# Optimization experiments

Hardware: AMD Instinct MI355X
Metric: run time of the kernel (lower is better)

Reference implementation:

```python
import jax, jax.numpy as jnp
import numpy as np

N_NODES = 100000
N_EDGES = 1600000
IN_C, HID_C, OUT_C = 128, 128, 64


def setup_inputs() -> dict:
    key = jax.random.key(0)
    ks = jax.random.split(key, 8)
    x = jax.random.normal(ks[0], (N_NODES, IN_C), dtype=jnp.float32)
    edge_index = jax.random.randint(ks[1], (2, N_EDGES), 0, N_NODES, dtype=jnp.int64)
    # SAGEConv params: lin_l (aggregated neighbors, with bias), lin_r (root, no bias)
    s1 = 1.0 / np.sqrt(IN_C)
    s2 = 1.0 / np.sqrt(HID_C)
    W1_l = jax.random.uniform(ks[2], (IN_C, HID_C), jnp.float32, -s1, s1)
    b1_l = jnp.zeros((HID_C,), jnp.float32)
    W1_r = jax.random.uniform(ks[3], (IN_C, HID_C), jnp.float32, -s1, s1)
    W2_l = jax.random.uniform(ks[4], (HID_C, OUT_C), jnp.float32, -s2, s2)
    b2_l = jnp.zeros((OUT_C,), jnp.float32)
    W2_r = jax.random.uniform(ks[5], (HID_C, OUT_C), jnp.float32, -s2, s2)
    return {"x": x, "edge_index": edge_index, "W1_l": W1_l, "b1_l": b1_l,
            "W1_r": W1_r, "W2_l": W2_l, "b2_l": b2_l, "W2_r": W2_r}


def _sage_conv(x, src, dst, W_l, b_l, W_r):
    # gather source features, scatter-max reduce onto destinations
    msg = x[src]                                             # [E, C]
    aggr = jax.ops.segment_max(msg, dst, num_segments=N_NODES)
    aggr = jnp.where(jnp.isfinite(aggr), aggr, 0.0)          # isolated nodes -> 0 (PyG behavior)
    return aggr @ W_l + b_l + x @ W_r


def reference(x, edge_index, W1_l, b1_l, W1_r, W2_l, b2_l, W2_r):
    src, dst = edge_index[0], edge_index[1]
    h = _sage_conv(x, src, dst, W1_l, b1_l, W1_r)
    h = jax.nn.relu(h)
    # dropout is identity in eval mode
    out = _sage_conv(h, src, dst, W2_l, b2_l, W2_r)
    return out
```

## Files before the change

kernel.cpp:

```cpp
#include <hip/hip_runtime.h>
#include <cstdint>

#define NNODES 100000
#define NEDGES 1600000
#define NBKT   196
#define CAP    9216
#define BIN_CHUNK 4096
#define GBIN ((NEDGES + BIN_CHUNK - 1) / BIN_CHUNK)
#define GCVT (NNODES * 16 / 256)
#define GWPK 24

typedef __attribute__((ext_vector_type(8))) __bf16 bf16x8;
typedef __attribute__((ext_vector_type(4))) float f32x4;
typedef short v2s __attribute__((ext_vector_type(2)));

__device__ __forceinline__ unsigned short f2bf_rne(float f) {
    unsigned int u = __float_as_uint(f);
    u += 0x7fffu + ((u >> 16) & 1u);
    return (unsigned short)(u >> 16);
}
__device__ __forceinline__ unsigned encdec(unsigned u) {
    return u ^ (((u & 0x80008000u) >> 15) * 0x7FFFu);
}
__device__ __forceinline__ unsigned pkmax(unsigned a, unsigned b) {
    v2s r = __builtin_elementwise_max(__builtin_bit_cast(v2s, a), __builtin_bit_cast(v2s, b));
    return __builtin_bit_cast(unsigned, r);
}
__device__ __forceinline__ uint4 pkmax4(uint4 a, uint4 b) {
    uint4 r;
    r.x = pkmax(a.x, b.x); r.y = pkmax(a.y, b.y);
    r.z = pkmax(a.z, b.z); r.w = pkmax(a.w, b.w);
    return r;
}


__global__ __launch_bounds__(256) void prep_kernel(
        const int* __restrict__ src, const int* __restrict__ dst,
        unsigned int* __restrict__ binArr, int* __restrict__ bucketFill,
        const float4* __restrict__ xin, uint4* __restrict__ xeout,
        const float* __restrict__ W1l, const float* __restrict__ W1r,
        const float* __restrict__ W2l, const float* __restrict__ W2r,
        uint4* __restrict__ Wf1, uint4* __restrict__ Wf2, int nE) {
    if (blockIdx.x >= GBIN + GCVT) {
        int t = (blockIdx.x - GBIN - GCVT) * 256 + threadIdx.x;
        unsigned short s[8];
        if (t < 4096) {
            int h = t >> 11, kt = (t >> 9) & 3, nt = (t >> 6) & 7, lane = t & 63;
            const float* W = h ? W1r : W1l;
            int k0 = kt * 32 + (lane >> 4) * 8;
            int col = nt * 16 + (lane & 15);
#pragma unroll
            for (int jj = 0; jj < 8; ++jj) s[jj] = f2bf_rne(W[(k0 + jj) * 128 + col]);
            uint4 o;
            o.x = (unsigned)s[0] | ((unsigned)s[1] << 16);
            o.y = (unsigned)s[2] | ((unsigned)s[3] << 16);
            o.z = (unsigned)s[4] | ((unsigned)s[5] << 16);
            o.w = (unsigned)s[6] | ((unsigned)s[7] << 16);
            Wf1[t] = o;
        } else {
            int u = t - 4096;
            int h = u >> 10, kt = (u >> 8) & 3, nt = (u >> 6) & 3, lane = u & 63;
            const float* W = h ? W2r : W2l;
            int k0 = kt * 32 + (lane >> 4) * 8;
            int col = nt * 16 + (lane & 15);
#pragma unroll
            for (int jj = 0; jj < 8; ++jj) s[jj] = f2bf_rne(W[(k0 + jj) * 64 + col]);
            uint4 o;
            o.x = (unsigned)s[0] | ((unsigned)s[1] << 16);
            o.y = (unsigned)s[2] | ((unsigned)s[3] << 16);
            o.z = (unsigned)s[4] | ((unsigned)s[5] << 16);
            o.w = (unsigned)s[6] | ((unsigned)s[7] << 16);
            Wf2[u] = o;
        }
        return;
    }
    if (blockIdx.x >= GBIN) {
        int t = (blockIdx.x - GBIN) * 256 + threadIdx.x;
        int s = t / (NNODES * 8);
        int rem = t - s * (NNODES * 8);
        int n = rem >> 3, j = rem & 7;
        int f = n * 32 + s * 16 + j * 2;
        float4 v0 = xin[f], v1 = xin[f + 1];
        uint4 o;
        o.x = encdec((unsigned)f2bf_rne(v0.x) | ((unsigned)f2bf_rne(v0.y) << 16));
        o.y = encdec((unsigned)f2bf_rne(v0.z) | ((unsigned)f2bf_rne(v0.w) << 16));
        o.z = encdec((unsigned)f2bf_rne(v1.x) | ((unsigned)f2bf_rne(v1.y) << 16));
        o.w = encdec((unsigned)f2bf_rne(v1.z) | ((unsigned)f2bf_rne(v1.w) << 16));
        xeout[t] = o;
        return;
    }
    __shared__ unsigned int stage[BIN_CHUNK];
    __shared__ unsigned char bof[BIN_CHUNK];
    __shared__ int cnt[256], cstart[256], gbase[256];
    const int tid = threadIdx.x;
    const int blockStart = blockIdx.x * BIN_CHUNK;
    const int chunkN = min(BIN_CHUNK, nE - blockStart);
    cnt[tid] = 0;
    __syncthreads();
    int myd[16], mys[16];
    unsigned short myo[16];
#pragma unroll
    for (int i = 0; i < 16; ++i) {
        int idx = i * 256 + tid;
        if (idx < chunkN) {
            myd[i] = dst[blockStart + idx];
            mys[i] = src[blockStart + idx];
            myo[i] = (unsigned short)atomicAdd(&cnt[myd[i] >> 9], 1);
        }
    }
    __syncthreads();
    int v = cnt[tid];
    for (int off = 1; off < 256; off <<= 1) {
        int add = (tid >= off) ? cnt[tid - off] : 0;
        __syncthreads();
        cnt[tid] += add;
        __syncthreads();
    }
    cstart[tid] = cnt[tid] - v;
    if (tid < NBKT && v > 0) gbase[tid] = atomicAdd(&bucketFill[tid], v);
    __syncthreads();
#pragma unroll
    for (int i = 0; i < 16; ++i) {
        int idx = i * 256 + tid;
        if (idx < chunkN) {
            int b = myd[i] >> 9;
            int p = cstart[b] + (int)myo[i];
            stage[p] = ((unsigned)(myd[i] & 511) << 17) | (unsigned)mys[i];
            bof[p] = (unsigned char)b;
        }
    }
    __syncthreads();
#pragma unroll
    for (int i = 0; i < 16; ++i) {
        int idx = i * 256 + tid;
        if (idx < chunkN) {
            int b = bof[idx];
            int slot = gbase[b] + (idx - cstart[b]);
            if (slot < CAP) binArr[(size_t)b * CAP + slot] = stage[idx];
        }
    }
}

__global__ __launch_bounds__(1024) void build_csr_kernel(
        const unsigned int* __restrict__ binArr, const int* __restrict__ bucketFill,
        unsigned int* __restrict__ sortedSrc,
        int* __restrict__ rowBeg, int* __restrict__ rowEnd) {
    __shared__ unsigned int stage[CAP];
    __shared__ unsigned short ordv[CAP];
    __shared__ int ncnt[512], nstart[512];
    const int b = blockIdx.x;
    const int t = threadIdx.x;
    const int cnt_b = min(bucketFill[b], CAP);
    if (t < 512) ncnt[t] = 0;
    __syncthreads();
    for (int i = t; i < cnt_b; i += 1024) {
        unsigned int e = binArr[(size_t)b * CAP + i];
        stage[i] = e;
        ordv[i] = (unsigned short)atomicAdd(&ncnt[e >> 17], 1);
    }
    __syncthreads();
    int v = (t < 512) ? ncnt[t] : 0;
    for (int off = 1; off < 512; off <<= 1) {
        int add = (t >= off && t < 512) ? ncnt[t - off] : 0;
        __syncthreads();
        if (t < 512) ncnt[t] += add;
        __syncthreads();
    }
    if (t < 512) {
        int start = ncnt[t] - v;
        nstart[t] = start;
        int n = (b << 9) + t;
        if (n < NNODES) {
            rowBeg[n] = b * CAP + start;
            rowEnd[n] = b * CAP + start + v;
        }
    }
    __syncthreads();
    for (int i = t; i < cnt_b; i += 1024) {
        unsigned int e = stage[i];
        sortedSrc[(size_t)b * CAP + nstart[e >> 17] + (int)ordv[i]] = e & 0x1FFFFu;
    }
}

template<int BN, bool RELU, bool ENCOUT, typename OutT>
__global__ __launch_bounds__(256) void sage_fused(
        const uint4* __restrict__ xsl,
        const int* __restrict__ rowBeg,
        const int* __restrict__ rowEnd,
        const unsigned int* __restrict__ sortedSrc,
        const uint4* __restrict__ Wf,
        const float* __restrict__ bias,
        OutT* __restrict__ C,
        int nN) {
    constexpr int NT = BN / 16;
    constexpr int NTW = BN / 64;
    __shared__ uint4 lds[16][17];
    const int wv   = threadIdx.x >> 6;
    const int lane = threadIdx.x & 63;
    const int n0   = blockIdx.x * 16;

    {
        const int s  = wv & 1;
        const int nh = wv >> 1;
        const int k  = lane >> 3;
        const int j  = lane & 7;
        const int kb = k << 3;
        const int n  = n0 + nh * 8 + k;
        const size_t srow = (size_t)s * nN;

        const int beg = rowBeg[n], end = rowEnd[n];
        const int m = end - beg;

        int maxm = m;
        maxm = max(maxm, __shfl_xor(maxm, 8));
        maxm = max(maxm, __shfl_xor(maxm, 16));
        maxm = max(maxm, __shfl_xor(maxm, 32));

        int idv0 = 0, idv1 = 0;
        if (m > 0) {
            idv0 = (int)sortedSrc[min(beg + j,     end - 1)];
            idv1 = (int)sortedSrc[min(beg + 8 + j, end - 1)];
        }
        int a0 = __shfl(idv0, kb | 0), a1 = __shfl(idv0, kb | 1);
        int a2 = __shfl(idv0, kb | 2), a3 = __shfl(idv0, kb | 3);
        int a4 = __shfl(idv0, kb | 4), a5 = __shfl(idv0, kb | 5);
        int a6 = __shfl(idv0, kb | 6), a7 = __shfl(idv0, kb | 7);
        int b0 = __shfl(idv1, kb | 0), b1 = __shfl(idv1, kb | 1);
        int b2 = __shfl(idv1, kb | 2), b3 = __shfl(idv1, kb | 3);
        int b4 = __shfl(idv1, kb | 4), b5 = __shfl(idv1, kb | 5);
        int b6 = __shfl(idv1, kb | 6), b7 = __shfl(idv1, kb | 7);
        uint4 q0  = xsl[(srow + a0) * 8 + j];
        uint4 q1  = xsl[(srow + a1) * 8 + j];
        uint4 q2  = xsl[(srow + a2) * 8 + j];
        uint4 q3  = xsl[(srow + a3) * 8 + j];
        uint4 q4  = xsl[(srow + a4) * 8 + j];
        uint4 q5  = xsl[(srow + a5) * 8 + j];
        uint4 q6  = xsl[(srow + a6) * 8 + j];
        uint4 q7  = xsl[(srow + a7) * 8 + j];
        uint4 q8  = xsl[(srow + b0) * 8 + j];
        uint4 q9  = xsl[(srow + b1) * 8 + j];
        uint4 q10 = xsl[(srow + b2) * 8 + j];
        uint4 q11 = xsl[(srow + b3) * 8 + j];
        uint4 q12 = xsl[(srow + b4) * 8 + j];
        uint4 q13 = xsl[(srow + b5) * 8 + j];
        uint4 q14 = xsl[(srow + b6) * 8 + j];
        uint4 q15 = xsl[(srow + b7) * 8 + j];
        uint4 accA = pkmax4(pkmax4(pkmax4(q0, q1), pkmax4(q2, q3)),
                            pkmax4(pkmax4(q4, q5), pkmax4(q6, q7)));
        uint4 accB = pkmax4(pkmax4(pkmax4(q8, q9), pkmax4(q10, q11)),
                            pkmax4(pkmax4(q12, q13), pkmax4(q14, q15)));
        uint4 acc = pkmax4(accA, accB);

        for (int e0 = 16; e0 < maxm; e0 += 8) {
            if (e0 < m) {
                int idt = (int)sortedSrc[min(beg + e0 + j, end - 1)];
                int t0 = __shfl(idt, kb | 0), t1 = __shfl(idt, kb | 1);
                int t2 = __shfl(idt, kb | 2), t3 = __shfl(idt, kb | 3);
                int t4 = __shfl(idt, kb | 4), t5 = __shfl(idt, kb | 5);
                int t6 = __shfl(idt, kb | 6), t7 = __shfl(idt, kb | 7);
                uint4 u0 = xsl[(srow + t0) * 8 + j];
                uint4 u1 = xsl[(srow + t1) * 8 + j];
                uint4 u2 = xsl[(srow + t2) * 8 + j];
                uint4 u3 = xsl[(srow + t3) * 8 + j];
                uint4 u4 = xsl[(srow + t4) * 8 + j];
                uint4 u5 = xsl[(srow + t5) * 8 + j];
                uint4 u6 = xsl[(srow + t6) * 8 + j];
                uint4 u7 = xsl[(srow + t7) * 8 + j];
                acc = pkmax4(acc, pkmax4(pkmax4(pkmax4(u0, u1), pkmax4(u2, u3)),
                                         pkmax4(pkmax4(u4, u5), pkmax4(u6, u7))));
            }
        }

        uint4 o;
        if (m > 0) { o = acc; }
        else       { o.x = o.y = o.z = o.w = 0u; }
        lds[nh * 8 + k][s * 8 + j] = o;
    }
    __syncthreads();

    const int quad = lane >> 4;
    const int mrow = lane & 15;
    const int r    = n0 + mrow;

    f32x4 acc[NTW];
#pragma unroll
    for (int t = 0; t < NTW; ++t) acc[t] = (f32x4){0.f, 0.f, 0.f, 0.f};

#pragma unroll
    for (int kt = 0; kt < 4; ++kt) {
        const int q = kt * 4 + quad;
        uint4 ta = lds[mrow][q];
        uint4 tr = xsl[((size_t)(q >> 3) * nN + r) * 8 + (q & 7)];
        ta.x = encdec(ta.x); ta.y = encdec(ta.y); ta.z = encdec(ta.z); ta.w = encdec(ta.w);
        tr.x = encdec(tr.x); tr.y = encdec(tr.y); tr.z = encdec(tr.z); tr.w = encdec(tr.w);
        bf16x8 aa = __builtin_bit_cast(bf16x8, ta);
        bf16x8 ar = __builtin_bit_cast(bf16x8, tr);
#pragma unroll
        for (int t = 0; t < NTW; ++t) {
            const int ct = wv * NTW + t;
            bf16x8 wb0 = __builtin_bit_cast(bf16x8, Wf[(kt * NT + ct) * 64 + lane]);
            acc[t] = __builtin_amdgcn_mfma_f32_16x16x32_bf16(aa, wb0, acc[t], 0, 0, 0);
            bf16x8 wb1 = __builtin_bit_cast(bf16x8, Wf[((4 + kt) * NT + ct) * 64 + lane]);
            acc[t] = __builtin_amdgcn_mfma_f32_16x16x32_bf16(ar, wb1, acc[t], 0, 0, 0);
        }
    }

#pragma unroll
    for (int t = 0; t < NTW; ++t) {
        const int col = (wv * NTW + t) * 16 + mrow;
        const float bv = bias[col];
#pragma unroll
        for (int rr = 0; rr < 4; ++rr) {
            const int grow = n0 + quad * 4 + rr;
            float v = acc[t][rr] + bv;
            if (RELU) v = fmaxf(v, 0.0f);
            if constexpr (ENCOUT) {
                unsigned u = f2bf_rne(v);
                u ^= ((u >> 15) & 1u) * 0x7FFFu;
                C[((size_t)(col >> 6) * nN + grow) * 64 + (col & 63)] = (OutT)u;
            } else {
                C[(size_t)grow * BN + col] = (OutT)v;
            }
        }
    }
}

extern "C" void kernel_launch(void* const* d_in, const int* in_sizes, int n_in,
                              void* d_out, int out_size, void* d_ws, size_t ws_size,
                              hipStream_t stream) {
    const float* x   = (const float*)d_in[0];
    const int*   ei  = (const int*)d_in[1];
    const float* W1l = (const float*)d_in[2];
    const float* b1l = (const float*)d_in[3];
    const float* W1r = (const float*)d_in[4];
    const float* W2l = (const float*)d_in[5];
    const float* b2l = (const float*)d_in[6];
    const float* W2r = (const float*)d_in[7];
    float* out = (float*)d_out;

    const int* src = ei;
    const int* dst = ei + NEDGES;

    char* ws = (char*)d_ws;
    unsigned short* xe    = (unsigned short*)ws; ws += (size_t)NNODES * 128 * 2;
    unsigned short* he    = (unsigned short*)ws; ws += (size_t)NNODES * 128 * 2;
    unsigned int* binArr    = (unsigned int*)ws; ws += (size_t)NBKT * CAP * 4;
    unsigned int* sortedSrc = (unsigned int*)ws; ws += (size_t)NBKT * CAP * 4;
    int* rowBeg     = (int*)ws; ws += (size_t)NNODES * 4;
    int* rowEnd     = (int*)ws; ws += (size_t)NNODES * 4;
    int* bucketFill = (int*)ws; ws += 256 * 4;
    uint4* Wf1 = (uint4*)ws; ws += 4096 * 16;
    uint4* Wf2 = (uint4*)ws; ws += 2048 * 16;

    const int gFus = NNODES / 16;

    hipMemsetAsync(bucketFill, 0, 256 * sizeof(int), stream);
    prep_kernel<<<GBIN + GCVT + GWPK, 256, 0, stream>>>(
        src, dst, binArr, bucketFill, (const float4*)x, (uint4*)xe,
        W1l, W1r, W2l, W2r, Wf1, Wf2, NEDGES);
    build_csr_kernel<<<NBKT, 1024, 0, stream>>>(binArr, bucketFill, sortedSrc, rowBeg, rowEnd);

    sage_fused<128, true, true, unsigned short><<<gFus, 256, 0, stream>>>(
        (const uint4*)xe, rowBeg, rowEnd, sortedSrc, Wf1, b1l, he, NNODES);
    sage_fused<64, false, false, float><<<gFus, 256, 0, stream>>>(
        (const uint4*)he, rowBeg, rowEnd, sortedSrc, Wf2, b2l, out, NNODES);
}
```

Baseline: 260.1 us.

## Make each wave own 16 nodes, aggregating directly into MFMA registers

Restructures the fused SAGE layer so each wavefront gathers neighbor max for 16 nodes with its lanes laid out to match the MFMA A-operand layout, removing the LDS staging and block barrier. Each wave then computes all output columns itself, and the grid shrinks to 64 nodes per block. This removes shared-memory traffic and synchronisation, at the cost of each wave loading the full weight set and a different gather access pattern (4 uint4 loads per neighbor per lane instead of 1).

```diff
diff --git a/kernel.cpp b/kernel.cpp
--- a/kernel.cpp
+++ b/kernel.cpp
@@ -30,6 +30,11 @@
     uint4 r;
     r.x = pkmax(a.x, b.x); r.y = pkmax(a.y, b.y);
     r.z = pkmax(a.z, b.z); r.w = pkmax(a.w, b.w);
+    return r;
+}
+__device__ __forceinline__ uint4 dec4(uint4 a) {
+    uint4 r;
+    r.x = encdec(a.x); r.y = encdec(a.y); r.z = encdec(a.z); r.w = encdec(a.w);
     return r;
 }
 
@@ -183,7 +188,7 @@
 }
 
 template<int BN, bool RELU, bool ENCOUT, typename OutT>
-__global__ __launch_bounds__(256) void sage_fused(
+__global__ __launch_bounds__(256) void sage_fused_bf(
         const uint4* __restrict__ xsl,
         const int* __restrict__ rowBeg,
         const int* __restrict__ rowEnd,
@@ -193,133 +198,135 @@
         OutT* __restrict__ C,
         int nN) {
     constexpr int NT = BN / 16;
-    constexpr int NTW = BN / 64;
-    __shared__ uint4 lds[16][17];
     const int wv   = threadIdx.x >> 6;
     const int lane = threadIdx.x & 63;
-    const int n0   = blockIdx.x * 16;
-
+    const int nd   = lane & 15;
+    const int fq   = lane >> 4;
+    const int nbase = blockIdx.x * 64 + wv * 16;
+    if (nbase >= nN) return;
+
+    const int n = min(nbase + nd, nN - 1);
+    const int beg = rowBeg[n], end = rowEnd[n];
+    const int m = end - beg;
+
+    int maxm = m;
+    maxm = max(maxm, __shfl_xor(maxm, 1));
+    maxm = max(maxm, __shfl_xor(maxm, 2));
+    maxm = max(maxm, __shfl_xor(maxm, 4));
+    maxm = max(maxm, __shfl_xor(maxm, 8));
+
+    const size_t c0 = (size_t)fq;
+    const size_t c1 = (size_t)(4 + fq);
+    const size_t c2 = (size_t)nN * 8 + fq;
+    const size_t c3 = (size_t)nN * 8 + 4 + fq;
+
+    int idv0 = 0, idv1 = 0, idv2 = 0, idv3 = 0;
+    if (m > 0) {
+        idv0 = (int)sortedSrc[min(beg + 0  + fq, end - 1)];
+        idv1 = (int)sortedSrc[min(beg + 4  + fq, end - 1)];
+        idv2 = (int)sortedSrc[min(beg + 8  + fq, end - 1)];
+        idv3 = (int)sortedSrc[min(beg + 12 + fq, end - 1)];
+    }
+
+    uint4 acc0, acc1, acc2, acc3;
     {
-        const int s  = wv & 1;
-        const int nh = wv >> 1;
-        const int k  = lane >> 3;
-        const int j  = lane & 7;
-        const int kb = k << 3;
-        const int n  = n0 + nh * 8 + k;
-        const size_t srow = (size_t)s * nN;
-
-        const int beg = rowBeg[n], end = rowEnd[n];
-        const int m = end - beg;
-
-        int maxm = m;
-        maxm = max(maxm, __shfl_xor(maxm, 8));
-        maxm = max(maxm, __shfl_xor(maxm, 16));
-        maxm = max(maxm, __shfl_xor(maxm, 32));
-
-        int idv0 = 0, idv1 = 0;
-        if (m > 0) {
-            idv0 = (int)sortedSrc[min(beg + j,     end - 1)];
-            idv1 = (int)sortedSrc[min(beg + 8 + j, end - 1)];
-        }
-        int a0 = __shfl(idv0, kb | 0), a1 = __shfl(idv0, kb | 1);
-        int a2 = __shfl(idv0, kb | 2), a3 = __shfl(idv0, kb | 3);
-        int a4 = __shfl(idv0, kb | 4), a5 = __shfl(idv0, kb | 5);
-        int a6 = __shfl(idv0, kb | 6), a7 = __shfl(idv0, kb | 7);
-        int b0 = __shfl(idv1, kb | 0), b1 = __shfl(idv1, kb | 1);
-        int b2 = __shfl(idv1, kb | 2), b3 = __shfl(idv1, kb | 3);
-        int b4 = __shfl(idv1, kb | 4), b5 = __shfl(idv1, kb | 5);
-        int b6 = __shfl(idv1, kb | 6), b7 = __shfl(idv1, kb | 7);
-        uint4 q0  = xsl[(srow + a0) * 8 + j];
-        uint4 q1  = xsl[(srow + a1) * 8 + j];
-        uint4 q2  = xsl[(srow + a2) * 8 + j];
-        uint4 q3  = xsl[(srow + a3) * 8 + j];
-        uint4 q4  = xsl[(srow + a4) * 8 + j];
-        uint4 q5  = xsl[(srow + a5) * 8 + j];
-        uint4 q6  = xsl[(srow + a6) * 8 + j];
-        uint4 q7  = xsl[(srow + a7) * 8 + j];
-        uint4 q8  = xsl[(srow + b0) * 8 + j];
-        uint4 q9  = xsl[(srow + b1) * 8 + j];
-        uint4 q10 = xsl[(srow + b2) * 8 + j];
-        uint4 q11 = xsl[(srow + b3) * 8 + j];
-        uint4 q12 = xsl[(srow + b4) * 8 + j];
-        uint4 q13 = xsl[(srow + b5) * 8 + j];
-        uint4 q14 = xsl[(srow + b6) * 8 + j];
-        uint4 q15 = xsl[(srow + b7) * 8 + j];
-        uint4 accA = pkmax4(pkmax4(pkmax4(q0, q1), pkmax4(q2, q3)),
-                            pkmax4(pkmax4(q4, q5), pkmax4(q6, q7)));
-        uint4 accB = pkmax4(pkmax4(pkmax4(q8, q9), pkmax4(q10, q11)),
-                            pkmax4(pkmax4(q12, q13), pkmax4(q14, q15)));
-        uint4 acc = pkmax4(accA, accB);
-
-        for (int e0 = 16; e0 < maxm; e0 += 8) {
-            if (e0 < m) {
-                int idt = (int)sortedSrc[min(beg + e0 + j, end - 1)];
-                int t0 = __shfl(idt, kb | 0), t1 = __shfl(idt, kb | 1);
-                int t2 = __shfl(idt, kb | 2), t3 = __shfl(idt, kb | 3);
-                int t4 = __shfl(idt, kb | 4), t5 = __shfl(idt, kb | 5);
-                int t6 = __shfl(idt, kb | 6), t7 = __shfl(idt, kb | 7);
-                uint4 u0 = xsl[(srow + t0) * 8 + j];
-                uint4 u1 = xsl[(srow + t1) * 8 + j];
-                uint4 u2 = xsl[(srow + t2) * 8 + j];
-                uint4 u3 = xsl[(srow + t3) * 8 + j];
-                uint4 u4 = xsl[(srow + t4) * 8 + j];
-                uint4 u5 = xsl[(srow + t5) * 8 + j];
-                uint4 u6 = xsl[(srow + t6) * 8 + j];
-                uint4 u7 = xsl[(srow + t7) * 8 + j];
-                acc = pkmax4(acc, pkmax4(pkmax4(pkmax4(u0, u1), pkmax4(u2, u3)),
-                                         pkmax4(pkmax4(u4, u5), pkmax4(u6, u7))));
-            }
-        }
-
-        uint4 o;
-        if (m > 0) { o = acc; }
-        else       { o.x = o.y = o.z = o.w = 0u; }
-        lds[nh * 8 + k][s * 8 + j] = o;
-    }
-    __syncthreads();
-
-    const int quad = lane >> 4;
-    const int mrow = lane & 15;
-    const int r    = n0 + mrow;
-
-    f32x4 acc[NTW];
-#pragma unroll
-    for (int t = 0; t < NTW; ++t) acc[t] = (f32x4){0.f, 0.f, 0.f, 0.f};
-
-#pragma unroll
-    for (int kt = 0; kt < 4; ++kt) {
-        const int q = kt * 4 + quad;
-        uint4 ta = lds[mrow][q];
-        uint4 tr = xsl[((size_t)(q >> 3) * nN + r) * 8 + (q & 7)];
-        ta.x = encdec(ta.x); ta.y = encdec(ta.y); ta.z = encdec(ta.z); ta.w = encdec(ta.w);
-        tr.x = encdec(tr.x); tr.y = encdec(tr.y); tr.z = encdec(tr.z); tr.w = encdec(tr.w);
-        bf16x8 aa = __builtin_bit_cast(bf16x8, ta);
-        bf16x8 ar = __builtin_bit_cast(bf16x8, tr);
-#pragma unroll
-        for (int t = 0; t < NTW; ++t) {
-            const int ct = wv * NTW + t;
-            bf16x8 wb0 = __builtin_bit_cast(bf16x8, Wf[(kt * NT + ct) * 64 + lane]);
-            acc[t] = __builtin_amdgcn_mfma_f32_16x16x32_bf16(aa, wb0, acc[t], 0, 0, 0);
-            bf16x8 wb1 = __builtin_bit_cast(bf16x8, Wf[((4 + kt) * NT + ct) * 64 + lane]);
-            acc[t] = __builtin_amdgcn_mfma_f32_16x16x32_bf16(ar, wb1, acc[t], 0, 0, 0);
-        }
-    }
-
-#pragma unroll
-    for (int t = 0; t < NTW; ++t) {
-        const int col = (wv * NTW + t) * 16 + mrow;
+        int e0 = __shfl(idv0, nd), e1 = __shfl(idv0, 16 + nd);
+        int e2 = __shfl(idv0, 32 + nd), e3 = __shfl(idv0, 48 + nd);
+        uint4 p00 = xsl[c0 + (size_t)e0 * 8], p10 = xsl[c0 + (size_t)e1 * 8];
+        uint4 p20 = xsl[c0 + (size_t)e2 * 8], p30 = xsl[c0 + (size_t)e3 * 8];
+        uint4 p01 = xsl[c1 + (size_t)e0 * 8], p11 = xsl[c1 + (size_t)e1 * 8];
+        uint4 p21 = xsl[c1 + (size_t)e2 * 8], p31 = xsl[c1 + (size_t)e3 * 8];
+        uint4 p02 = xsl[c2 + (size_t)e0 * 8], p12 = xsl[c2 + (size_t)e1 * 8];
+        uint4 p22 = xsl[c2 + (size_t)e2 * 8], p32 = xsl[c2 + (size_t)e3 * 8];
+        uint4 p03 = xsl[c3 + (size_t)e0 * 8], p13 = xsl[c3 + (size_t)e1 * 8];
+        uint4 p23 = xsl[c3 + (size_t)e2 * 8], p33 = xsl[c3 + (size_t)e3 * 8];
+        acc0 = pkmax4(pkmax4(p00, p10), pkmax4(p20, p30));
+        acc1 = pkmax4(pkmax4(p01, p11), pkmax4(p21, p31));
+        acc2 = pkmax4(pkmax4(p02, p12), pkmax4(p22, p32));
+        acc3 = pkmax4(pkmax4(p03, p13), pkmax4(p23, p33));
+    }
+#define BATCH_ACC(idv)                                                         \
+    {                                                                          \
+        int e0 = __shfl(idv, nd), e1 = __shfl(idv, 16 + nd);                   \
+        int e2 = __shfl(idv, 32 + nd), e3 = __shfl(idv, 48 + nd);              \
+        uint4 p00 = xsl[c0 + (size_t)e0 * 8], p10 = xsl[c0 + (size_t)e1 * 8];  \
+        uint4 p20 = xsl[c0 + (size_t)e2 * 8], p30 = xsl[c0 + (size_t)e3 * 8];  \
+        uint4 p01 = xsl[c1 + (size_t)e0 * 8], p11 = xsl[c1 + (size_t)e1 * 8];  \
+        uint4 p21 = xsl[c1 + (size_t)e2 * 8], p31 = xsl[c1 + (size_t)e3 * 8];  \
+        uint4 p02 = xsl[c2 + (size_t)e0 * 8], p12 = xsl[c2 + (size_t)e1 * 8];  \
+        uint4 p22 = xsl[c2 + (size_t)e2 * 8], p32 = xsl[c2 + (size_t)e3 * 8];  \
+        uint4 p03 = xsl[c3 + (size_t)e0 * 8], p13 = xsl[c3 + (size_t)e1 * 8];  \
+        uint4 p23 = xsl[c3 + (size_t)e2 * 8], p33 = xsl[c3 + (size_t)e3 * 8];  \
+        acc0 = pkmax4(acc0, pkmax4(pkmax4(p00, p10), pkmax4(p20, p30)));       \
+        acc1 = pkmax4(acc1, pkmax4(pkmax4(p01, p11), pkmax4(p21, p31)));       \
+        acc2 = pkmax4(acc2, pkmax4(pkmax4(p02, p12), pkmax4(p22, p32)));       \
+        acc3 = pkmax4(acc3, pkmax4(pkmax4(p03, p13), pkmax4(p23, p33)));       \
+    }
+    BATCH_ACC(idv1);
+    BATCH_ACC(idv2);
+    BATCH_ACC(idv3);
+
+    for (int eb = 16; eb < maxm; eb += 4) {
+        if (eb < m) {
+            int idt = (int)sortedSrc[min(beg + eb + fq, end - 1)];
+            BATCH_ACC(idt);
+        }
+    }
+#undef BATCH_ACC
+
+    if (m == 0) {
+        acc0 = (uint4){0, 0, 0, 0}; acc1 = acc0; acc2 = acc0; acc3 = acc0;
+    }
+
+    uint4 tr0 = xsl[c0 + (size_t)n * 8];
+    uint4 tr1 = xsl[c1 + (size_t)n * 8];
+    uint4 tr2 = xsl[c2 + (size_t)n * 8];
+    uint4 tr3 = xsl[c3 + (size_t)n * 8];
+
+    bf16x8 aa0 = __builtin_bit_cast(bf16x8, dec4(acc0));
+    bf16x8 aa1 = __builtin_bit_cast(bf16x8, dec4(acc1));
+    bf16x8 aa2 = __builtin_bit_cast(bf16x8, dec4(acc2));
+    bf16x8 aa3 = __builtin_bit_cast(bf16x8, dec4(acc3));
+    bf16x8 ar0 = __builtin_bit_cast(bf16x8, dec4(tr0));
+    bf16x8 ar1 = __builtin_bit_cast(bf16x8, dec4(tr1));
+    bf16x8 ar2 = __builtin_bit_cast(bf16x8, dec4(tr2));
+    bf16x8 ar3 = __builtin_bit_cast(bf16x8, dec4(tr3));
+
+#pragma unroll
+    for (int nt = 0; nt < NT; ++nt) {
+        f32x4 cacc = (f32x4){0.f, 0.f, 0.f, 0.f};
+        cacc = __builtin_amdgcn_mfma_f32_16x16x32_bf16(
+            aa0, __builtin_bit_cast(bf16x8, Wf[(0 * NT + nt) * 64 + lane]), cacc, 0, 0, 0);
+        cacc = __builtin_amdgcn_mfma_f32_16x16x32_bf16(
+            aa1, __builtin_bit_cast(bf16x8, Wf[(1 * NT + nt) * 64 + lane]), cacc, 0, 0, 0);
+        cacc = __builtin_amdgcn_mfma_f32_16x16x32_bf16(
+            aa2, __builtin_bit_cast(bf16x8, Wf[(2 * NT + nt) * 64 + lane]), cacc, 0, 0, 0);
+        cacc = __builtin_amdgcn_mfma_f32_16x16x32_bf16(
+            aa3, __builtin_bit_cast(bf16x8, Wf[(3 * NT + nt) * 64 + lane]), cacc, 0, 0, 0);
+        cacc = __builtin_amdgcn_mfma_f32_16x16x32_bf16(
+            ar0, __builtin_bit_cast(bf16x8, Wf[(4 * NT + nt) * 64 + lane]), cacc, 0, 0, 0);
+        cacc = __builtin_amdgcn_mfma_f32_16x16x32_bf16(
+            ar1, __builtin_bit_cast(bf16x8, Wf[(5 * NT + nt) * 64 + lane]), cacc, 0, 0, 0);
+        cacc = __builtin_amdgcn_mfma_f32_16x16x32_bf16(
+            ar2, __builtin_bit_cast(bf16x8, Wf[(6 * NT + nt) * 64 + lane]), cacc, 0, 0, 0);
+        cacc = __builtin_amdgcn_mfma_f32_16x16x32_bf16(
+            ar3, __builtin_bit_cast(bf16x8, Wf[(7 * NT + nt) * 64 + lane]), cacc, 0, 0, 0);
+
+        const int col = nt * 16 + nd;
         const float bv = bias[col];
 #pragma unroll
         for (int rr = 0; rr < 4; ++rr) {
-            const int grow = n0 + quad * 4 + rr;
-            float v = acc[t][rr] + bv;
-            if (RELU) v = fmaxf(v, 0.0f);
-            if constexpr (ENCOUT) {
-                unsigned u = f2bf_rne(v);
-                u ^= ((u >> 15) & 1u) * 0x7FFFu;
-                C[((size_t)(col >> 6) * nN + grow) * 64 + (col & 63)] = (OutT)u;
-            } else {
-                C[(size_t)grow * BN + col] = (OutT)v;
+            const int grow = nbase + fq * 4 + rr;
+            if (grow < nN) {
+                float vv = cacc[rr] + bv;
+                if (RELU) vv = fmaxf(vv, 0.0f);
+                if constexpr (ENCOUT) {
+                    unsigned u = f2bf_rne(vv);
+                    u ^= ((u >> 15) & 1u) * 0x7FFFu;
+                    C[((size_t)(col >> 6) * nN + grow) * 64 + (col & 63)] = (OutT)u;
+                } else {
+                    C[(size_t)grow * BN + col] = (OutT)vv;
+                }
             }
         }
     }
@@ -352,7 +359,7 @@
     uint4* Wf1 = (uint4*)ws; ws += 4096 * 16;
     uint4* Wf2 = (uint4*)ws; ws += 2048 * 16;
 
-    const int gFus = NNODES / 16;
+    const int gFus = (NNODES + 63) / 64;
 
     hipMemsetAsync(bucketFill, 0, 256 * sizeof(int), stream);
     prep_kernel<<<GBIN + GCVT + GWPK, 256, 0, stream>>>(
@@ -360,8 +367,8 @@
         W1l, W1r, W2l, W2r, Wf1, Wf2, NEDGES);
     build_csr_kernel<<<NBKT, 1024, 0, stream>>>(binArr, bucketFill, sortedSrc, rowBeg, rowEnd);
 
-    sage_fused<128, true, true, unsigned short><<<gFus, 256, 0, stream>>>(
+    sage_fused_bf<128, true, true, unsigned short><<<gFus, 256, 0, stream>>>(
         (const uint4*)xe, rowBeg, rowEnd, sortedSrc, Wf1, b1l, he, NNODES);
-    sage_fused<64, false, false, float><<<gFus, 256, 0, stream>>>(
+    sage_fused_bf<64, false, false, float><<<gFus, 256, 0, stream>>>(
         (const uint4*)he, rowBeg, rowEnd, sortedSrc, Wf2, b2l, out, NNODES);
 }
```

New measurement: 306.4 us. 17.8% more time.
